# Kernel tuning notes

Hardware: AMD Instinct MI355X
Metric: run time of the kernel (lower is better)

The kernel has to match this reference:

```python
import jax, jax.numpy as jnp
import numpy as np

V, E, HL, HH, T_STEPS, N_STEPS = 32000, 768, 1024, 768, 5, 3
B, S = 8, 256
EPS = 1e-5


def _ln(x, g, b):
    m = jnp.mean(x, axis=-1, keepdims=True)
    v = jnp.var(x, axis=-1, keepdims=True)
    return (x - m) * jax.lax.rsqrt(v + EPS) * g + b


def _gru(x, h, Wi, bi, Wh, bh, lni_g, lni_b, lnh_g, lnh_b):
    # Wi: [3, in_dim, H]; gates stacked in order (r, z, n)
    xi = jnp.einsum('bd,kdh->kbh', x, Wi) + bi[:, None, :]
    hi = jnp.einsum('bh,khg->kbg', h, Wh) + bh[:, None, :]
    xi = _ln(xi, lni_g[:, None, :], lni_b[:, None, :])
    hi = _ln(hi, lnh_g[:, None, :], lnh_b[:, None, :])
    r = jax.nn.sigmoid(xi[0] + hi[0])
    z = jax.nn.sigmoid(xi[1] + hi[1])
    n = jnp.tanh(xi[2] + r * hi[2])
    return (1.0 - z) * n + z * h


def setup_inputs() -> dict:
    key = jax.random.key(0)
    ks = jax.random.split(key, 12)
    lin = E + HH  # low-level cell input dim (x concat h_h)

    def xavier(k, shape, fan_in, fan_out):
        lim = float(np.sqrt(6.0 / (fan_in + fan_out)))
        return jax.random.uniform(k, shape, jnp.float32, -lim, lim)

    inp = {
        'input_ids': jax.random.randint(ks[0], (B, S), 0, V),
        'emb': xavier(ks[1], (V, E), V, E),
        'ln_emb_g': jnp.ones((E,), jnp.float32),
        'ln_emb_b': jnp.zeros((E,), jnp.float32),
        'low_Wi': xavier(ks[2], (3, lin, HL), lin, HL),
        'low_bi': jnp.zeros((3, HL), jnp.float32),
        'low_Wh': xavier(ks[3], (3, HL, HL), HL, HL),
        'low_bh': jnp.zeros((3, HL), jnp.float32),
        'low_lni_g': jnp.ones((3, HL), jnp.float32),
        'low_lni_b': jnp.zeros((3, HL), jnp.float32),
        'low_lnh_g': jnp.ones((3, HL), jnp.float32),
        'low_lnh_b': jnp.zeros((3, HL), jnp.float32),
        'high_Wi': xavier(ks[4], (3, HL, HH), HL, HH),
        'high_bi': jnp.zeros((3, HH), jnp.float32),
        'high_Wh': xavier(ks[5], (3, HH, HH), HH, HH),
        'high_bh': jnp.zeros((3, HH), jnp.float32),
        'high_lni_g': jnp.ones((3, HH), jnp.float32),
        'high_lni_b': jnp.zeros((3, HH), jnp.float32),
        'high_lnh_g': jnp.ones((3, HH), jnp.float32),
        'high_lnh_b': jnp.zeros((3, HH), jnp.float32),
        'Wout': xavier(ks[6], (HH, V), HH, V),
        'bout': jnp.zeros((V,), jnp.float32),
    }
    return inp


def reference(input_ids, emb, ln_emb_g, ln_emb_b,
              low_Wi, low_bi, low_Wh, low_bh,
              low_lni_g, low_lni_b, low_lnh_g, low_lnh_b,
              high_Wi, high_bi, high_Wh, high_bh,
              high_lni_g, high_lni_b, high_lnh_g, high_lnh_b,
              Wout, bout):
    b = input_ids.shape[0]
    h_l0 = jnp.zeros((b, HL), jnp.float32)
    h_h0 = jnp.zeros((b, HH), jnp.float32)

    def step(carry, ids_t):
        h_l, h_h = carry
        x = _ln(emb[ids_t], ln_emb_g, ln_emb_b)  # [B, E]
        for _ in range(N_STEPS):
            for _ in range(T_STEPS):
                h_l = _gru(jnp.concatenate([x, h_h], axis=-1), h_l,
                           low_Wi, low_bi, low_Wh, low_bh,
                           low_lni_g, low_lni_b, low_lnh_g, low_lnh_b)
            h_h = _gru(h_l, h_h,
                       high_Wi, high_bi, high_Wh, high_bh,
                       high_lni_g, high_lni_b, high_lnh_g, high_lnh_b)
        logits_t = h_h @ Wout + bout  # [B, V]
        return (h_l, h_h), logits_t

    _, logits = jax.lax.scan(step, (h_l0, h_h0), input_ids.T)  # [S, B, V]
    return jnp.transpose(logits, (1, 0, 2))  # [B, S, V]
```

## Files before the change

kernel.cpp:

```cpp
#include <hip/hip_runtime.h>
#include <hip/hip_bf16.h>


#define NWG 128
#define NTH 256
#define EPSV 1e-5f
#define NROUND 4608

typedef __attribute__((ext_vector_type(4))) float f32x4;
typedef __attribute__((ext_vector_type(8))) short short8;
typedef unsigned long long u64;

struct PArgs {
  const int* ids; const float* emb; const float* lng; const float* lnb;
  const float* lWi; const float* lbi; const float* lWh; const float* lbh;
  const float* llig; const float* llib; const float* llhg; const float* llhb;
  const float* hWi; const float* hbi; const float* hWh; const float* hbh;
  const float* hlig; const float* hlib; const float* hlhg; const float* hlhb;
  int* arr; int* rel; int* cnt; u64* sredG; u64* statsG; float* hlR; float* hhR;
  __hip_bfloat16* hist; float* WiT; float* hWiT; float* hWhT;
};

__device__ __forceinline__ float sigm(float x) { return 1.f / (1.f + __expf(-x)); }
__device__ __forceinline__ float tanh_f(float x) {
  x = fminf(15.f, fmaxf(-15.f, x));
  float e = __expf(2.f * x);
  return (e - 1.f) / (e + 1.f);
}
__device__ __forceinline__ int aldi(const int* p) {
  return __hip_atomic_load(p, __ATOMIC_RELAXED, __HIP_MEMORY_SCOPE_AGENT);
}
__device__ __forceinline__ u64 aldu(const u64* p) {
  return __hip_atomic_load(p, __ATOMIC_RELAXED, __HIP_MEMORY_SCOPE_AGENT);
}
__device__ __forceinline__ void asti(int* p, int v) {
  __hip_atomic_store(p, v, __ATOMIC_RELAXED, __HIP_MEMORY_SCOPE_AGENT);
}
__device__ __forceinline__ u64 pk2(float a, float b) {
  union { u64 u; float f[2]; } c; c.f[0] = a; c.f[1] = b; return c.u;
}
__device__ __forceinline__ void astu(u64* p, u64 v) {
  __hip_atomic_store(p, v, __ATOMIC_RELAXED, __HIP_MEMORY_SCOPE_AGENT);
}
__device__ __forceinline__ void ast(float* p, float v) {
  __hip_atomic_store(p, v, __ATOMIC_RELAXED, __HIP_MEMORY_SCOPE_AGENT);
}
__device__ __forceinline__ void ald4x8(const float* p0, const float* p1,
                                       const float* p2, const float* p3,
                                       const float* p4, const float* p5,
                                       const float* p6, const float* p7,
                                       float4& a, float4& b, float4& c, float4& d,
                                       float4& e, float4& f, float4& g, float4& h) {
  asm volatile(
      "global_load_dwordx4 %0, %8, off sc1\n\t"
      "global_load_dwordx4 %1, %9, off sc1\n\t"
      "global_load_dwordx4 %2, %10, off sc1\n\t"
      "global_load_dwordx4 %3, %11, off sc1\n\t"
      "global_load_dwordx4 %4, %12, off sc1\n\t"
      "global_load_dwordx4 %5, %13, off sc1\n\t"
      "global_load_dwordx4 %6, %14, off sc1\n\t"
      "global_load_dwordx4 %7, %15, off sc1\n\t"
      "s_waitcnt vmcnt(0)"
      : "=&v"(a), "=&v"(b), "=&v"(c), "=&v"(d),
        "=&v"(e), "=&v"(f), "=&v"(g), "=&v"(h)
      : "v"(p0), "v"(p1), "v"(p2), "v"(p3),
        "v"(p4), "v"(p5), "v"(p6), "v"(p7)
      : "memory");
}
__device__ __forceinline__ void ald4x6(const float* p0, const float* p1,
                                       const float* p2, const float* p3,
                                       const float* p4, const float* p5,
                                       float4& a, float4& b, float4& c,
                                       float4& d, float4& e, float4& f) {
  asm volatile(
      "global_load_dwordx4 %0, %6, off sc1\n\t"
      "global_load_dwordx4 %1, %7, off sc1\n\t"
      "global_load_dwordx4 %2, %8, off sc1\n\t"
      "global_load_dwordx4 %3, %9, off sc1\n\t"
      "global_load_dwordx4 %4, %10, off sc1\n\t"
      "global_load_dwordx4 %5, %11, off sc1\n\t"
      "s_waitcnt vmcnt(0)"
      : "=&v"(a), "=&v"(b), "=&v"(c), "=&v"(d), "=&v"(e), "=&v"(f)
      : "v"(p0), "v"(p1), "v"(p2), "v"(p3), "v"(p4), "v"(p5)
      : "memory");
}

__global__ void __launch_bounds__(NTH) hrm_recur(PArgs P) {
  __shared__ float WhS[24 * 1024];
  __shared__ float Bb[8 * 1024];
  __shared__ float Bh[8 * 768];
  __shared__ float XW[24 * 8];
  __shared__ float xiNs[24 * 8];
  __shared__ float stg[2 * 24 * 8];
  __shared__ float sred[96];
  __shared__ float xm[8], xrs[8];
  __shared__ float mbuf[96][4];
  __shared__ int idsh[8];
  __shared__ int okf;

  const int tid = threadIdx.x;

  if (blockIdx.x >= NWG) {
    const int pl = blockIdx.x - NWG;
    #pragma unroll 1
    for (int r = 1; r <= NROUND; ++r) {
      if (tid < 64) {
        const u64* ap = (const u64*)(P.arr + pl * 128) + tid;
        int lim = 1 << 22, g1 = 1;
        for (;;) {
          u64 v = aldu(ap);
          int a0 = (int)(unsigned)(v & 0xffffffffull);
          int a1 = (int)(unsigned)(v >> 32);
          if (__all(a0 >= r && a1 >= r)) break;
          if (--lim == 0) { g1 = 0; break; }
          __builtin_amdgcn_s_sleep(1);
        }
        if (tid == 0) okf = g1;
      }
      __syncthreads();
      if (!okf) {
        if (tid < 8) asti(P.rel + pl * 128 + tid * 16, 1 << 30);
        return;
      }
      const int ph = (r - 1) % 6;
      const bool full = (ph == 0 || ph == 5);
      const int lo = pl * 24 + (full ? 0 : 12);
      const int n  = full ? 24 : 12;
      const float invD = (ph == 5) ? (1.f / 768.f) : (1.f / 1024.f);
      const int par = r & 1;
      if (tid < (n >> 1) * 8) {
        int rp = (lo >> 1) + (tid >> 3), q = tid & 7;
        const float* fb = (const float*)(P.statsG + (size_t)par * 128 * 48);
        float4 s; s.x = 0.f; s.y = 0.f; s.z = 0.f; s.w = 0.f;
        #pragma unroll
        for (int blk = 0; blk < 2; ++blk) {
          int w0 = q * 16 + blk * 8;
          float4 t0,t1,t2,t3,t4,t5,t6,t7;
          ald4x8(fb + (size_t)(w0+0)*96 + rp*4, fb + (size_t)(w0+1)*96 + rp*4,
                 fb + (size_t)(w0+2)*96 + rp*4, fb + (size_t)(w0+3)*96 + rp*4,
                 fb + (size_t)(w0+4)*96 + rp*4, fb + (size_t)(w0+5)*96 + rp*4,
                 fb + (size_t)(w0+6)*96 + rp*4, fb + (size_t)(w0+7)*96 + rp*4,
                 t0,t1,t2,t3,t4,t5,t6,t7);
          s.x += t0.x+t1.x+t2.x+t3.x+t4.x+t5.x+t6.x+t7.x;
          s.y += t0.y+t1.y+t2.y+t3.y+t4.y+t5.y+t6.y+t7.y;
          s.z += t0.z+t1.z+t2.z+t3.z+t4.z+t5.z+t6.z+t7.z;
          s.w += t0.w+t1.w+t2.w+t3.w+t4.w+t5.w+t6.w+t7.w;
        }
        mbuf[tid][0] = s.x; mbuf[tid][1] = s.y; mbuf[tid][2] = s.z; mbuf[tid][3] = s.w;
      }
      __syncthreads();
      if (tid < n) {
        int rpl = tid >> 1, comp = tid & 1;
        float s1 = 0.f, s2 = 0.f;
        #pragma unroll
        for (int q = 0; q < 8; ++q) {
          s1 += mbuf[rpl * 8 + q][comp * 2 + 0];
          s2 += mbuf[rpl * 8 + q][comp * 2 + 1];
        }
        float m = s1 * invD;
        float rs = rsqrtf(s2 * invD - m * m + EPSV);
        astu(P.sredG + (size_t)pl * 96 + (size_t)par * 48 + lo + tid, pk2(m, rs));
      }
      asm volatile("s_waitcnt vmcnt(0)" ::: "memory");
      __syncthreads();
      if (tid < 8) asti(P.rel + pl * 128 + tid * 16, r);
    }
    return;
  }

  const int wg = blockIdx.x;
  const int ks = tid & 31, cg = tid >> 5;
  const int lj8 = wg * 8, lj6 = wg * 6;
  const int rep = wg & 3;

  auto arriveA = [&](int pl, int r) {
    asm volatile("s_waitcnt vmcnt(0)" ::: "memory");
    __syncthreads();
    if (tid == 0) asti(P.arr + pl * 128 + wg, r);
  };
  auto pollRel = [&](int pl, int r, bool full) -> bool {
    if (tid == 0) {
      const int* rp = P.rel + pl * 128 + (wg & 7) * 16;
      int lim = 1 << 22, v = 0;
      do {
        v = aldi(rp);
        if (v >= r) break;
        __builtin_amdgcn_s_sleep(1);
      } while (--lim);
      okf = (lim != 0 && v < (1 << 29)) ? 1 : 0;
    }
    __syncthreads();
    if (okf) {
      int lo = pl * 24 + (full ? 0 : 12);
      int n  = full ? 24 : 12;
      if (tid < n) {
        int row = lo + tid;
        union { u64 u; float f[2]; } c;
        c.u = aldu(P.sredG + (size_t)pl * 96 + (size_t)(r & 1) * 48 + row);
        int local = row - pl * 24;
        int set = local / 12, rem = local % 12, g = rem >> 2, bq = rem & 3;
        int b = pl * 4 + bq;
        sred[set * 48 + g * 16 + b * 2] = c.f[0];
        sred[set * 48 + g * 16 + b * 2 + 1] = c.f[1];
      }
      __syncthreads();
    }
    return okf != 0;
  };
  auto waitAB = [&](int target) -> bool {
    if (tid < 64) {
      bool active = tid < 16;
      int pl = (tid >> 3) & 1, idx = tid & 7;
      const int* cp = P.cnt + (active ? (pl * 256 + idx * 32) : 0);
      int lim = 1 << 22;
      for (;;) {
        int v = active ? aldi(cp) : 0;
        v += __shfl_xor(v, 1);
        v += __shfl_xor(v, 2);
        v += __shfl_xor(v, 4);
        int sumA = __shfl(v, 0);
        int sumB = __shfl(v, 8);
        if (sumA >= target && sumB >= target) break;
        if (--lim == 0) break;
        __builtin_amdgcn_s_sleep(2);
      }
      if (tid == 0) okf = (lim != 0) ? 1 : 0;
    }
    __syncthreads();
    return okf != 0;
  };
  auto gate_commit = [&](int pl) {
    asm volatile("s_waitcnt vmcnt(0)" ::: "memory");
    if (tid == 0)
      __hip_atomic_fetch_add(P.cnt + pl * 256 + (size_t)(wg & 7) * 32, 1,
                             __ATOMIC_RELAXED, __HIP_MEMORY_SCOPE_AGENT);
  };

  auto stage_all_hl = [&]() {
    const float* base = P.hlR + (size_t)rep * 8192 + tid * 4;
    float4 t0,t1,t2,t3,t4,t5,t6,t7;
    ald4x8(base + 0*1024, base + 1*1024, base + 2*1024, base + 3*1024,
           base + 4*1024, base + 5*1024, base + 6*1024, base + 7*1024,
           t0,t1,t2,t3,t4,t5,t6,t7);
    float* db = &Bb[tid * 4];
    *(float4*)&db[0*1024] = t0; *(float4*)&db[1*1024] = t1;
    *(float4*)&db[2*1024] = t2; *(float4*)&db[3*1024] = t3;
    *(float4*)&db[4*1024] = t4; *(float4*)&db[5*1024] = t5;
    *(float4*)&db[6*1024] = t6; *(float4*)&db[7*1024] = t7;
  };
  auto stage_all_hh = [&]() {
    const float* base = P.hhR + (size_t)rep * 6144;
    int bi[6], ki[6];
    #pragma unroll
    for (int i = 0; i < 6; ++i) {
      int c = i * 256 + tid; int bq = c / 192; int k = (c - bq * 192) * 4;
      bi[i] = bq; ki[i] = k;
    }
    float4 t0,t1,t2,t3,t4,t5;
    ald4x6(base + bi[0]*768 + ki[0], base + bi[1]*768 + ki[1],
           base + bi[2]*768 + ki[2], base + bi[3]*768 + ki[3],
           base + bi[4]*768 + ki[4], base + bi[5]*768 + ki[5],
           t0,t1,t2,t3,t4,t5);
    *(float4*)&Bh[bi[0]*768 + ki[0]] = t0; *(float4*)&Bh[bi[1]*768 + ki[1]] = t1;
    *(float4*)&Bh[bi[2]*768 + ki[2]] = t2; *(float4*)&Bh[bi[3]*768 + ki[3]] = t3;
    *(float4*)&Bh[bi[4]*768 + ki[4]] = t4; *(float4*)&Bh[bi[5]*768 + ki[5]] = t5;
  };

  auto gemm_lowh = [&](int pl, float (&acc)[3][4]) {
    const int c0 = cg * 3;
    const float* w0p = &WhS[(c0 + 0) * 1024];
    const float* w1p = &WhS[(c0 + 1) * 1024];
    const float* w2p = &WhS[(c0 + 2) * 1024];
    const float* hb = &Bb[pl * 4096];
    #pragma unroll
    for (int i = 0; i < 8; ++i) {
      int k = i * 128 + ks * 4;
      float4 w0 = *(const float4*)&w0p[k];
      float4 w1 = *(const float4*)&w1p[k];
      float4 w2 = *(const float4*)&w2p[k];
      #pragma unroll
      for (int bq = 0; bq < 4; ++bq) {
        float4 h = *(const float4*)&hb[bq * 1024 + k];
        acc[0][bq] += w0.x*h.x + w0.y*h.y + w0.z*h.z + w0.w*h.w;
        acc[1][bq] += w1.x*h.x + w1.y*h.y + w1.z*h.z + w1.w*h.w;
        acc[2][bq] += w2.x*h.x + w2.y*h.y + w2.z*h.z + w2.w*h.w;
      }
    }
  };
  auto gemm_xih = [&](int pl, float (&acc)[3][4]) {
    const float* wp[3];
    #pragma unroll
    for (int cc = 0; cc < 3; ++cc) {
      int c = cg * 3 + cc; int g = c >> 3, jj = c & 7;
      wp[cc] = P.WiT + ((size_t)g * 1024 + lj8 + jj) * 1536 + 768;
    }
    const float* hb = &Bh[pl * 3072];
    #pragma unroll
    for (int i = 0; i < 6; ++i) {
      int k = i * 128 + ks * 4;
      float4 w0 = *(const float4*)&wp[0][k];
      float4 w1 = *(const float4*)&wp[1][k];
      float4 w2 = *(const float4*)&wp[2][k];
      #pragma unroll
      for (int bq = 0; bq < 4; ++bq) {
        float4 h = *(const float4*)&hb[bq * 768 + k];
        acc[0][bq] += w0.x*h.x + w0.y*h.y + w0.z*h.z + w0.w*h.w;
        acc[1][bq] += w1.x*h.x + w1.y*h.y + w1.z*h.z + w1.w*h.w;
        acc[2][bq] += w2.x*h.x + w2.y*h.y + w2.z*h.z + w2.w*h.w;
      }
    }
  };
  auto gemm_hxi = [&](int pl, float (&acc)[3][4]) {
    if (cg >= 6) return;
    const float* wp[3];
    #pragma unroll
    for (int cc = 0; cc < 3; ++cc) {
      int c = cg * 3 + cc; int g = c / 6, jj = c % 6;
      wp[cc] = P.hWiT + ((size_t)g * 768 + lj6 + jj) * 1024;
    }
    const float* hb = &Bb[pl * 4096];
    #pragma unroll
    for (int i = 0; i < 8; ++i) {
      int k = i * 128 + ks * 4;
      float4 w0 = *(const float4*)&wp[0][k];
      float4 w1 = *(const float4*)&wp[1][k];
      float4 w2 = *(const float4*)&wp[2][k];
      #pragma unroll
      for (int bq = 0; bq < 4; ++bq) {
        float4 h = *(const float4*)&hb[bq * 1024 + k];
        acc[0][bq] += w0.x*h.x + w0.y*h.y + w0.z*h.z + w0.w*h.w;
        acc[1][bq] += w1.x*h.x + w1.y*h.y + w1.z*h.z + w1.w*h.w;
        acc[2][bq] += w2.x*h.x + w2.y*h.y + w2.z*h.z + w2.w*h.w;
      }
    }
  };
  auto gemm_hhh = [&](int pl, float (&acc)[3][4]) {
    if (cg >= 6) return;
    const float* wp[3];
    #pragma unroll
    for (int cc = 0; cc < 3; ++cc) {
      int c = cg * 3 + cc; int g = c / 6, jj = c % 6;
      wp[cc] = P.hWhT + ((size_t)g * 768 + lj6 + jj) * 768;
    }
    const float* hb = &Bh[pl * 3072];
    #pragma unroll
    for (int i = 0; i < 6; ++i) {
      int k = i * 128 + ks * 4;
      float4 w0 = *(const float4*)&wp[0][k];
      float4 w1 = *(const float4*)&wp[1][k];
      float4 w2 = *(const float4*)&wp[2][k];
      #pragma unroll
      for (int bq = 0; bq < 4; ++bq) {
        float4 h = *(const float4*)&hb[bq * 768 + k];
        acc[0][bq] += w0.x*h.x + w0.y*h.y + w0.z*h.z + w0.w*h.w;
        acc[1][bq] += w1.x*h.x + w1.y*h.y + w1.z*h.z + w1.w*h.w;
        acc[2][bq] += w2.x*h.x + w2.y*h.y + w2.z*h.z + w2.w*h.w;
      }
    }
  };

  auto redstage = [&](int pl, float (&acc)[3][4], int set, const float* bias,
                      int dim, int perg, int jb, bool addXW) {
    #pragma unroll
    for (int cc = 0; cc < 3; ++cc)
      #pragma unroll
      for (int bq = 0; bq < 4; ++bq) {
        float v = acc[cc][bq];
        #pragma unroll
        for (int m = 1; m < 32; m <<= 1) v += __shfl_xor(v, m, 64);
        acc[cc][bq] = v;
      }
    if ((tid & 31) == 0) {
      int cgl = tid >> 5;
      #pragma unroll
      for (int cc = 0; cc < 3; ++cc) {
        int c = cgl * 3 + cc;
        if (c < perg * 3) {
          int g = (perg == 8) ? (c >> 3) : (c / 6);
          int jj = (perg == 8) ? (c & 7) : (c % 6);
          float bs = bias[g * dim + jb + jj];
          #pragma unroll
          for (int bq = 0; bq < 4; ++bq) {
            float v = acc[cc][bq] + bs;
            if (addXW) v += XW[c * 8 + pl * 4 + bq];
            stg[set * 192 + c * 8 + pl * 4 + bq] = v;
          }
        }
      }
    }
  };

  auto stats_put = [&](int pl, int par, int set, int perg) {
    if (tid < 12) {
      int g = tid >> 2, bq = tid & 3;
      float s1 = 0.f, s2 = 0.f;
      for (int jj = 0; jj < perg; ++jj) {
        float v = stg[set * 192 + (g * perg + jj) * 8 + pl * 4 + bq];
        s1 += v; s2 += v * v;
      }
      int row = pl * 24 + set * 12 + g * 4 + bq;
      astu(P.statsG + ((size_t)par * 128 + wg) * 48 + row, pk2(s1, s2));
    }
  };

  auto gate_low = [&](int pl, bool isA) {
    if (tid < 32) {
      int jj = tid & 7, bq = tid >> 3; int b = pl * 4 + bq; int j = lj8 + jj;
      float xin[3], hin[3];
      #pragma unroll
      for (int g = 0; g < 3; ++g) {
        int c = g * 8 + jj;
        if (isA) {
          float m = sred[g * 16 + b * 2], rs = sred[g * 16 + b * 2 + 1];
          float v = (stg[c * 8 + b] - m) * rs * P.llig[g * 1024 + j] + P.llib[g * 1024 + j];
          xiNs[c * 8 + b] = v; xin[g] = v;
        } else {
          xin[g] = xiNs[c * 8 + b];
        }
        float m2 = sred[48 + g * 16 + b * 2], rs2 = sred[48 + g * 16 + b * 2 + 1];
        hin[g] = (stg[192 + c * 8 + b] - m2) * rs2 * P.llhg[g * 1024 + j] + P.llhb[g * 1024 + j];
      }
      float rg = sigm(xin[0] + hin[0]);
      float zg = sigm(xin[1] + hin[1]);
      float ng = tanh_f(xin[2] + rg * hin[2]);
      float hold = Bb[b * 1024 + j];
      float hv = (1.f - zg) * ng + zg * hold;
      #pragma unroll
      for (int rp = 0; rp < 4; ++rp) ast(&P.hlR[rp * 8192 + b * 1024 + j], hv);
    }
  };

  auto gate_high = [&](int pl, int t, int nn) {
    if (tid < 24) {
      int jj = tid % 6, bq = tid / 6; int b = pl * 4 + bq; int j = lj6 + jj;
      float xin[3], hin[3];
      #pragma unroll
      for (int g = 0; g < 3; ++g) {
        int c = g * 6 + jj;
        float m = sred[g * 16 + b * 2], rs = sred[g * 16 + b * 2 + 1];
        xin[g] = (stg[c * 8 + b] - m) * rs * P.hlig[g * 768 + j] + P.hlib[g * 768 + j];
        float m2 = sred[48 + g * 16 + b * 2], rs2 = sred[48 + g * 16 + b * 2 + 1];
        hin[g] = (stg[192 + c * 8 + b] - m2) * rs2 * P.hlhg[g * 768 + j] + P.hlhb[g * 768 + j];
      }
      float rg = sigm(xin[0] + hin[0]);
      float zg = sigm(xin[1] + hin[1]);
      float ng = tanh_f(xin[2] + rg * hin[2]);
      float hold = Bh[b * 768 + j];
      float hv = (1.f - zg) * ng + zg * hold;
      #pragma unroll
      for (int rp = 0; rp < 4; ++rp) ast(&P.hhR[rp * 6144 + b * 768 + j], hv);
      if (nn == 2) P.hist[((size_t)t * 8 + b) * 768 + j] = __float2bfloat16(hv);
    }
  };

  auto xfun = [&](int tt) {
    int bq = tid >> 5, u = tid & 31;
    if (tid < 8) idsh[tid] = P.ids[tid * 256 + tt];
    int id = P.ids[bq * 256 + tt];
    const float* e = P.emb + (size_t)id * 768;
    float s1 = 0.f, s2 = 0.f;
    #pragma unroll
    for (int q = 0; q < 24; q += 4) {
      float4 v = *(const float4*)&e[u * 24 + q];
      s1 += v.x + v.y + v.z + v.w;
      s2 += v.x*v.x + v.y*v.y + v.z*v.z + v.w*v.w;
    }
    #pragma unroll
    for (int m = 1; m < 32; m <<= 1) { s1 += __shfl_xor(s1, m, 64); s2 += __shfl_xor(s2, m, 64); }
    if (u == 0) { float mm = s1 / 768.f; xm[bq] = mm; xrs[bq] = rsqrtf(s2 / 768.f - mm * mm + EPSV); }
    __syncthreads();
    float acc[3][8] = {};
    const float* wp[3];
    #pragma unroll
    for (int cc = 0; cc < 3; ++cc) {
      int c = cg * 3 + cc; int g = c >> 3, jj = c & 7;
      wp[cc] = P.WiT + ((size_t)g * 1024 + lj8 + jj) * 1536;
    }
    int idv[8];
    #pragma unroll
    for (int bb = 0; bb < 8; ++bb) idv[bb] = idsh[bb];
    #pragma unroll
    for (int i = 0; i < 6; ++i) {
      int k = i * 128 + ks * 4;
      float4 w0 = *(const float4*)&wp[0][k];
      float4 w1 = *(const float4*)&wp[1][k];
      float4 w2 = *(const float4*)&wp[2][k];
      float4 gam = *(const float4*)&P.lng[k];
      float4 bet = *(const float4*)&P.lnb[k];
      #pragma unroll
      for (int bb = 0; bb < 8; ++bb) {
        float4 xv = *(const float4*)&P.emb[(size_t)idv[bb] * 768 + k];
        float4 xn;
        xn.x = (xv.x - xm[bb]) * xrs[bb] * gam.x + bet.x;
        xn.y = (xv.y - xm[bb]) * xrs[bb] * gam.y + bet.y;
        xn.z = (xv.z - xm[bb]) * xrs[bb] * gam.z + bet.z;
        xn.w = (xv.w - xm[bb]) * xrs[bb] * gam.w + bet.w;
        acc[0][bb] += w0.x*xn.x + w0.y*xn.y + w0.z*xn.z + w0.w*xn.w;
        acc[1][bb] += w1.x*xn.x + w1.y*xn.y + w1.z*xn.z + w1.w*xn.w;
        acc[2][bb] += w2.x*xn.x + w2.y*xn.y + w2.z*xn.z + w2.w*xn.w;
      }
    }
    #pragma unroll
    for (int cc = 0; cc < 3; ++cc)
      #pragma unroll
      for (int bb = 0; bb < 8; ++bb) {
        float v = acc[cc][bb];
        #pragma unroll
        for (int m = 1; m < 32; m <<= 1) v += __shfl_xor(v, m, 64);
        acc[cc][bb] = v;
      }
    if ((tid & 31) == 0) {
      int cgl = tid >> 5;
      #pragma unroll
      for (int cc = 0; cc < 3; ++cc)
        #pragma unroll
        for (int bb = 0; bb < 8; ++bb)
          XW[(cgl * 3 + cc) * 8 + bb] = acc[cc][bb];
    }
    __syncthreads();
  };

  #pragma unroll 1
  for (int g = 0; g < 3; ++g)
    for (int it = 0; it < 6; ++it) {
      int k = it * 256 + tid;
      const float* src = P.lWi + ((size_t)g * 1536 + k) * 1024 + lj8;
      float4 v0 = *(const float4*)src; float4 v1 = *(const float4*)(src + 4);
      float vv[8] = {v0.x, v0.y, v0.z, v0.w, v1.x, v1.y, v1.z, v1.w};
      for (int jj = 0; jj < 8; ++jj)
        P.WiT[((size_t)g * 1024 + lj8 + jj) * 1536 + k] = vv[jj];
    }
  #pragma unroll 1
  for (int g = 0; g < 3; ++g)
    for (int it = 0; it < 4; ++it) {
      int k = it * 256 + tid;
      const float* src = P.hWi + ((size_t)g * 1024 + k) * 768 + lj6;
      float2 a = *(const float2*)src, b2v = *(const float2*)(src + 2), c2v = *(const float2*)(src + 4);
      float vv[6] = {a.x, a.y, b2v.x, b2v.y, c2v.x, c2v.y};
      for (int jj = 0; jj < 6; ++jj)
        P.hWiT[((size_t)g * 768 + lj6 + jj) * 1024 + k] = vv[jj];
    }
  #pragma unroll 1
  for (int g = 0; g < 3; ++g)
    for (int it = 0; it < 3; ++it) {
      int k = it * 256 + tid;
      const float* src = P.hWh + ((size_t)g * 768 + k) * 768 + lj6;
      float2 a = *(const float2*)src, b2v = *(const float2*)(src + 2), c2v = *(const float2*)(src + 4);
      float vv[6] = {a.x, a.y, b2v.x, b2v.y, c2v.x, c2v.y};
      for (int jj = 0; jj < 6; ++jj)
        P.hWhT[((size_t)g * 768 + lj6 + jj) * 768 + k] = vv[jj];
    }
  #pragma unroll 1
  for (int g = 0; g < 3; ++g)
    for (int it = 0; it < 4; ++it) {
      int k = it * 256 + tid;
      const float* src = P.lWh + ((size_t)g * 1024 + k) * 1024 + lj8;
      float4 v0 = *(const float4*)src; float4 v1 = *(const float4*)(src + 4);
      float vv[8] = {v0.x, v0.y, v0.z, v0.w, v1.x, v1.y, v1.z, v1.w};
      for (int jj = 0; jj < 8; ++jj) WhS[(g * 8 + jj) * 1024 + k] = vv[jj];
    }
  __syncthreads();
  xfun(0);

  int r = 1;
  bool alive = true;
  #pragma unroll 1
  for (int t = 0; t < 256 && alive; ++t) {
    #pragma unroll 1
    for (int nn = 0; nn < 3 && alive; ++nn) {
      {
        alive = waitAB(NWG * (r - 1)); if (!alive) break;
        stage_all_hh(); stage_all_hl();
        __syncthreads();
        #pragma unroll 1
        for (int pl = 0; pl < 2; ++pl) {
          float aX[3][4] = {};
          gemm_xih(pl, aX);
          redstage(pl, aX, 0, P.lbi, 1024, 8, lj8, true);
          float aH[3][4] = {};
          gemm_lowh(pl, aH);
          redstage(pl, aH, 1, P.lbh, 1024, 8, lj8, false);
          __syncthreads();
          stats_put(pl, r & 1, 0, 8); stats_put(pl, r & 1, 1, 8);
          arriveA(pl, r);
        }
        #pragma unroll 1
        for (int pl = 0; pl < 2; ++pl) {
          alive = pollRel(pl, r, true); if (!alive) break;
          gate_low(pl, true);
          gate_commit(pl);
        }
        if (!alive) break;
        ++r;
      }
      #pragma unroll 1
      for (int it = 1; it < 5 && alive; ++it) {
        alive = waitAB(NWG * (r - 1)); if (!alive) break;
        stage_all_hl();
        __syncthreads();
        #pragma unroll 1
        for (int pl = 0; pl < 2; ++pl) {
          float a2[3][4] = {};
          gemm_lowh(pl, a2);
          redstage(pl, a2, 1, P.lbh, 1024, 8, lj8, false);
          __syncthreads();
          stats_put(pl, r & 1, 1, 8);
          arriveA(pl, r);
        }
        #pragma unroll 1
        for (int pl = 0; pl < 2; ++pl) {
          alive = pollRel(pl, r, false); if (!alive) break;
          gate_low(pl, false);
          gate_commit(pl);
        }
        if (!alive) break;
        ++r;
      }
      if (!alive) break;
      {
        alive = waitAB(NWG * (r - 1)); if (!alive) break;
        stage_all_hl(); stage_all_hh();
        __syncthreads();
        #pragma unroll 1
        for (int pl = 0; pl < 2; ++pl) {
          float aX[3][4] = {};
          gemm_hxi(pl, aX);
          redstage(pl, aX, 0, P.hbi, 768, 6, lj6, false);
          float aH[3][4] = {};
          gemm_hhh(pl, aH);
          redstage(pl, aH, 1, P.hbh, 768, 6, lj6, false);
          __syncthreads();
          stats_put(pl, r & 1, 0, 6); stats_put(pl, r & 1, 1, 6);
          arriveA(pl, r);
        }
        #pragma unroll 1
        for (int pl = 0; pl < 2; ++pl) {
          alive = pollRel(pl, r, true); if (!alive) break;
          gate_high(pl, t, nn);
          gate_commit(pl);
        }
        if (!alive) break;
        ++r;
        if (nn == 2 && t < 255) { __syncthreads(); xfun(t + 1); }
      }
    }
  }
}

__global__ void __launch_bounds__(256) wout_t(const float* __restrict__ W,
                                              __hip_bfloat16* __restrict__ WT) {
  __shared__ float T[64][65];
  int n0 = blockIdx.x * 64, k0 = blockIdx.y * 64;
  int tid = threadIdx.x;
  int lane16 = tid & 15, grp = tid >> 4;
  #pragma unroll
  for (int i = 0; i < 4; ++i) {
    int kl = i * 16 + grp; int nl = lane16 * 4;
    float4 v = *(const float4*)&W[(size_t)(k0 + kl) * 32000 + n0 + nl];
    T[kl][nl] = v.x; T[kl][nl + 1] = v.y; T[kl][nl + 2] = v.z; T[kl][nl + 3] = v.w;
  }
  __syncthreads();
  #pragma unroll
  for (int i = 0; i < 4; ++i) {
    int nl = i * 16 + grp; int kl = lane16 * 4;
    union { ushort4 v; __hip_bfloat16 h[4]; } u;
    for (int q = 0; q < 4; ++q) u.h[q] = __float2bfloat16(T[kl + q][nl]);
    *(ushort4*)&WT[(size_t)(n0 + nl) * 768 + k0 + kl] = u.v;
  }
}

__global__ void __launch_bounds__(256) logits_gemm(const __hip_bfloat16* __restrict__ Ah,
                                                   const __hip_bfloat16* __restrict__ Bt,
                                                   const float* __restrict__ bias,
                                                   float* __restrict__ out) {
  __shared__ short As[128 * 64];
  __shared__ short Bs[128 * 64];
  int m0 = blockIdx.y * 128, n0 = blockIdx.x * 128;
  int tid = threadIdx.x, lane = tid & 63, w = tid >> 6;
  int wr = w >> 1, wc = w & 1;
  int r16 = lane & 15, khalf = (lane >> 4) * 8;
  f32x4 acc[4][4];
  #pragma unroll
  for (int i = 0; i < 4; ++i)
    #pragma unroll
    for (int j = 0; j < 4; ++j)
      #pragma unroll
      for (int q = 0; q < 4; ++q) acc[i][j][q] = 0.f;

  for (int kt = 0; kt < 12; ++kt) {
    int k0 = kt * 64;
    __syncthreads();
    #pragma unroll
    for (int it = 0; it < 4; ++it) {
      int f = it * 2048 + tid * 8; int row = f >> 6, col = f & 63;
      *(uint4*)&As[f] = *(const uint4*)&Ah[(size_t)(m0 + row) * 768 + k0 + col];
      *(uint4*)&Bs[f] = *(const uint4*)&Bt[(size_t)(n0 + row) * 768 + k0 + col];
    }
    __syncthreads();
    #pragma unroll
    for (int kk = 0; kk < 64; kk += 32) {
      short8 af[4], bfr[4];
      #pragma unroll
      for (int i = 0; i < 4; ++i)
        af[i] = *(short8*)&As[(wr * 64 + i * 16 + r16) * 64 + kk + khalf];
      #pragma unroll
      for (int j = 0; j < 4; ++j)
        bfr[j] = *(short8*)&Bs[(wc * 64 + j * 16 + r16) * 64 + kk + khalf];
      #pragma unroll
      for (int i = 0; i < 4; ++i)
        #pragma unroll
        for (int j = 0; j < 4; ++j)
          acc[i][j] = __builtin_amdgcn_mfma_f32_16x16x32_bf16(af[i], bfr[j], acc[i][j], 0, 0, 0);
    }
  }
  #pragma unroll
  for (int i = 0; i < 4; ++i)
    #pragma unroll
    for (int j = 0; j < 4; ++j)
      #pragma unroll
      for (int q = 0; q < 4; ++q) {
        int m = m0 + wr * 64 + i * 16 + ((lane >> 4) * 4 + q);
        int n = n0 + wc * 64 + j * 16 + (lane & 15);
        out[(size_t)(m & 7) * 8192000 + (size_t)(m >> 3) * 32000 + n] =
            acc[i][j][q] + bias[n];
      }
}

extern "C" void kernel_launch(void* const* d_in, const int* in_sizes, int n_in,
                              void* d_out, int out_size, void* d_ws, size_t ws_size,
                              hipStream_t stream) {
  (void)in_sizes; (void)n_in; (void)out_size; (void)ws_size;
  char* wsb = (char*)d_ws;
  size_t off = 0;
  auto take = [&](size_t bytes) -> void* {
    void* p = wsb + off;
    off += (bytes + 1023) & ~(size_t)1023;
    return p;
  };
  int* arr    = (int*)take((size_t)2 * 128 * 4);
  int* rel    = (int*)take((size_t)2 * 128 * 4);
  int* cnt    = (int*)take((size_t)2 * 8 * 32 * 4);
  u64* sredG  = (u64*)take((size_t)2 * 2 * 48 * 8);
  float* hlR  = (float*)take((size_t)4 * 8 * 1024 * 4);
  float* hhR  = (float*)take((size_t)4 * 8 * 768 * 4);
  size_t state_bytes = off;
  u64* statsG = (u64*)take((size_t)2 * 128 * 48 * 8);
  __hip_bfloat16* hist = (__hip_bfloat16*)take((size_t)2048 * 768 * 2);
  float* WiT  = (float*)take((size_t)3 * 1024 * 1536 * 4);
  float* hWiT = (float*)take((size_t)3 * 768 * 1024 * 4);
  float* hWhT = (float*)take((size_t)3 * 768 * 768 * 4);
  __hip_bfloat16* WoutT = (__hip_bfloat16*)take((size_t)32000 * 768 * 2);

  hipMemsetAsync(d_ws, 0, state_bytes, stream);

  wout_t<<<dim3(500, 12), 256, 0, stream>>>((const float*)d_in[20], WoutT);

  PArgs A;
  A.ids = (const int*)d_in[0];   A.emb = (const float*)d_in[1];
  A.lng = (const float*)d_in[2]; A.lnb = (const float*)d_in[3];
  A.lWi = (const float*)d_in[4]; A.lbi = (const float*)d_in[5];
  A.lWh = (const float*)d_in[6]; A.lbh = (const float*)d_in[7];
  A.llig = (const float*)d_in[8];  A.llib = (const float*)d_in[9];
  A.llhg = (const float*)d_in[10]; A.llhb = (const float*)d_in[11];
  A.hWi = (const float*)d_in[12];  A.hbi = (const float*)d_in[13];
  A.hWh = (const float*)d_in[14];  A.hbh = (const float*)d_in[15];
  A.hlig = (const float*)d_in[16]; A.hlib = (const float*)d_in[17];
  A.hlhg = (const float*)d_in[18]; A.hlhb = (const float*)d_in[19];
  A.arr = arr; A.rel = rel; A.cnt = cnt; A.sredG = sredG; A.statsG = statsG;
  A.hlR = hlR; A.hhR = hhR;
  A.hist = hist; A.WiT = WiT; A.hWiT = hWiT; A.hWhT = hWhT;

  hrm_recur<<<NWG + 2, NTH, 0, stream>>>(A);

  logits_gemm<<<dim3(250, 16), 256, 0, stream>>>(hist, WoutT,
                                                 (const float*)d_in[21],
                                                 (float*)d_out);
}
```

Before: 60.28 ms.

## Merge per-half release polls and commits; widen stats reduction parallelism

Worker workgroups now poll both half-batch release flags at once and read both sets of LN stats together, then run both gate passes before a single combined commit, instead of alternating poll/gate/commit per half. The stats-reducer blocks use twice as many threads, each doing one 8-way load batch instead of two serial batches. The waitAB sleep interval is shortened. This aims to cut serialized synchronization latency on the recurrent critical path. The cost is losing overlap between the first half's gates and the second half's release, and adding slightly more polling traffic.

After: 67.79 ms. +12.5%, slower.

```diff
diff --git a/kernel.cpp b/kernel.cpp
--- a/kernel.cpp
+++ b/kernel.cpp
@@ -94,7 +94,7 @@
   __shared__ float stg[2 * 24 * 8];
   __shared__ float sred[96];
   __shared__ float xm[8], xrs[8];
-  __shared__ float mbuf[96][4];
+  __shared__ float mbuf[192][4];
   __shared__ int idsh[8];
   __shared__ int okf;
 
@@ -128,34 +128,29 @@
       const int n  = full ? 24 : 12;
       const float invD = (ph == 5) ? (1.f / 768.f) : (1.f / 1024.f);
       const int par = r & 1;
-      if (tid < (n >> 1) * 8) {
-        int rp = (lo >> 1) + (tid >> 3), q = tid & 7;
+      if (tid < (n >> 1) * 16) {
+        int rp = (lo >> 1) + (tid >> 4), q = tid & 15;
         const float* fb = (const float*)(P.statsG + (size_t)par * 128 * 48);
-        float4 s; s.x = 0.f; s.y = 0.f; s.z = 0.f; s.w = 0.f;
-        #pragma unroll
-        for (int blk = 0; blk < 2; ++blk) {
-          int w0 = q * 16 + blk * 8;
-          float4 t0,t1,t2,t3,t4,t5,t6,t7;
-          ald4x8(fb + (size_t)(w0+0)*96 + rp*4, fb + (size_t)(w0+1)*96 + rp*4,
-                 fb + (size_t)(w0+2)*96 + rp*4, fb + (size_t)(w0+3)*96 + rp*4,
-                 fb + (size_t)(w0+4)*96 + rp*4, fb + (size_t)(w0+5)*96 + rp*4,
-                 fb + (size_t)(w0+6)*96 + rp*4, fb + (size_t)(w0+7)*96 + rp*4,
-                 t0,t1,t2,t3,t4,t5,t6,t7);
-          s.x += t0.x+t1.x+t2.x+t3.x+t4.x+t5.x+t6.x+t7.x;
-          s.y += t0.y+t1.y+t2.y+t3.y+t4.y+t5.y+t6.y+t7.y;
-          s.z += t0.z+t1.z+t2.z+t3.z+t4.z+t5.z+t6.z+t7.z;
-          s.w += t0.w+t1.w+t2.w+t3.w+t4.w+t5.w+t6.w+t7.w;
-        }
-        mbuf[tid][0] = s.x; mbuf[tid][1] = s.y; mbuf[tid][2] = s.z; mbuf[tid][3] = s.w;
+        int w0 = q * 8;
+        float4 t0,t1,t2,t3,t4,t5,t6,t7;
+        ald4x8(fb + (size_t)(w0+0)*96 + rp*4, fb + (size_t)(w0+1)*96 + rp*4,
+               fb + (size_t)(w0+2)*96 + rp*4, fb + (size_t)(w0+3)*96 + rp*4,
+               fb + (size_t)(w0+4)*96 + rp*4, fb + (size_t)(w0+5)*96 + rp*4,
+               fb + (size_t)(w0+6)*96 + rp*4, fb + (size_t)(w0+7)*96 + rp*4,
+               t0,t1,t2,t3,t4,t5,t6,t7);
+        mbuf[tid][0] = t0.x+t1.x+t2.x+t3.x+t4.x+t5.x+t6.x+t7.x;
+        mbuf[tid][1] = t0.y+t1.y+t2.y+t3.y+t4.y+t5.y+t6.y+t7.y;
+        mbuf[tid][2] = t0.z+t1.z+t2.z+t3.z+t4.z+t5.z+t6.z+t7.z;
+        mbuf[tid][3] = t0.w+t1.w+t2.w+t3.w+t4.w+t5.w+t6.w+t7.w;
       }
       __syncthreads();
       if (tid < n) {
         int rpl = tid >> 1, comp = tid & 1;
         float s1 = 0.f, s2 = 0.f;
         #pragma unroll
-        for (int q = 0; q < 8; ++q) {
-          s1 += mbuf[rpl * 8 + q][comp * 2 + 0];
-          s2 += mbuf[rpl * 8 + q][comp * 2 + 1];
+        for (int q = 0; q < 16; ++q) {
+          s1 += mbuf[rpl * 16 + q][comp * 2 + 0];
+          s2 += mbuf[rpl * 16 + q][comp * 2 + 1];
         }
         float m = s1 * invD;
         float rs = rsqrtf(s2 * invD - m * m + EPSV);
@@ -178,23 +173,28 @@
     __syncthreads();
     if (tid == 0) asti(P.arr + pl * 128 + wg, r);
   };
-  auto pollRel = [&](int pl, int r, bool full) -> bool {
-    if (tid == 0) {
-      const int* rp = P.rel + pl * 128 + (wg & 7) * 16;
-      int lim = 1 << 22, v = 0;
-      do {
-        v = aldi(rp);
-        if (v >= r) break;
+  auto pollRelBoth = [&](int r, bool full) -> bool {
+    if (tid < 64) {
+      bool active = tid < 2;
+      const int* rp = P.rel + (active ? (tid * 128 + (wg & 7) * 16) : 0);
+      int lim = 1 << 22, v = 1 << 28;
+      for (;;) {
+        if (active) v = aldi(rp);
+        bool done = !active || (v >= r);
+        if (__all(done)) break;
+        if (--lim == 0) break;
         __builtin_amdgcn_s_sleep(1);
-      } while (--lim);
-      okf = (lim != 0 && v < (1 << 29)) ? 1 : 0;
+      }
+      int bad = (active && v >= (1 << 29)) ? 1 : 0;
+      bad = __any(bad) ? 1 : 0;
+      if (tid == 0) okf = (lim != 0 && !bad) ? 1 : 0;
     }
     __syncthreads();
     if (okf) {
-      int lo = pl * 24 + (full ? 0 : 12);
-      int n  = full ? 24 : 12;
-      if (tid < n) {
-        int row = lo + tid;
+      int per = full ? 24 : 12;
+      if (tid < per * 2) {
+        int pl = tid / per, i = tid % per;
+        int row = pl * 24 + (full ? 0 : 12) + i;
         union { u64 u; float f[2]; } c;
         c.u = aldu(P.sredG + (size_t)pl * 96 + (size_t)(r & 1) * 48 + row);
         int local = row - pl * 24;
@@ -222,18 +222,21 @@
         int sumB = __shfl(v, 8);
         if (sumA >= target && sumB >= target) break;
         if (--lim == 0) break;
-        __builtin_amdgcn_s_sleep(2);
+        __builtin_amdgcn_s_sleep(1);
       }
       if (tid == 0) okf = (lim != 0) ? 1 : 0;
     }
     __syncthreads();
     return okf != 0;
   };
-  auto gate_commit = [&](int pl) {
+  auto commit_both = [&]() {
     asm volatile("s_waitcnt vmcnt(0)" ::: "memory");
-    if (tid == 0)
-      __hip_atomic_fetch_add(P.cnt + pl * 256 + (size_t)(wg & 7) * 32, 1,
+    if (tid == 0) {
+      __hip_atomic_fetch_add(P.cnt + (size_t)(wg & 7) * 32, 1,
                              __ATOMIC_RELAXED, __HIP_MEMORY_SCOPE_AGENT);
+      __hip_atomic_fetch_add(P.cnt + 256 + (size_t)(wg & 7) * 32, 1,
+                             __ATOMIC_RELAXED, __HIP_MEMORY_SCOPE_AGENT);
+    }
   };
 
   auto stage_all_hl = [&]() {
@@ -584,13 +587,9 @@
           stats_put(pl, r & 1, 0, 8); stats_put(pl, r & 1, 1, 8);
           arriveA(pl, r);
         }
-        #pragma unroll 1
-        for (int pl = 0; pl < 2; ++pl) {
-          alive = pollRel(pl, r, true); if (!alive) break;
-          gate_low(pl, true);
-          gate_commit(pl);
-        }
-        if (!alive) break;
+        alive = pollRelBoth(r, true); if (!alive) break;
+        gate_low(0, true); gate_low(1, true);
+        commit_both();
         ++r;
       }
       #pragma unroll 1
@@ -607,13 +606,9 @@
           stats_put(pl, r & 1, 1, 8);
           arriveA(pl, r);
         }
-        #pragma unroll 1
-        for (int pl = 0; pl < 2; ++pl) {
-          alive = pollRel(pl, r, false); if (!alive) break;
-          gate_low(pl, false);
-          gate_commit(pl);
-        }
-        if (!alive) break;
+        alive = pollRelBoth(r, false); if (!alive) break;
+        gate_low(0, false); gate_low(1, false);
+        commit_both();
         ++r;
       }
       if (!alive) break;
@@ -633,13 +628,9 @@
           stats_put(pl, r & 1, 0, 6); stats_put(pl, r & 1, 1, 6);
           arriveA(pl, r);
         }
-        #pragma unroll 1
-        for (int pl = 0; pl < 2; ++pl) {
-          alive = pollRel(pl, r, true); if (!alive) break;
-          gate_high(pl, t, nn);
-          gate_commit(pl);
-        }
-        if (!alive) break;
+        alive = pollRelBoth(r, true); if (!alive) break;
+        gate_high(0, t, nn); gate_high(1, t, nn);
+        commit_both();
         ++r;
         if (nn == 2 && t < 255) { __syncthreads(); xfun(t + 1); }
       }
```
